# Performance work log

Hardware: AMD Instinct MI355X
Metric: run time of the kernel (lower is better)

## Reference

```python
import jax, jax.numpy as jnp
import numpy as np
from math import sqrt

B, C, L = 32, 32, 512            # batch, channels(enc_in), seq_len
INTRA, INTER = 1024, 256          # memory-bank intra_len, inter_len
DCP, DDE = 64, 512                # compress width (retrieved set size), denoise hidden
SCALE = 0.05


def setup_inputs() -> dict:
    key = jax.random.key(0)
    ks = jax.random.split(key, 12)
    s = 0.02  # small init scale for weights
    return {
        "x_loc": jax.random.normal(ks[0], (B, C, L), jnp.float32),
        "indices": jax.random.randint(ks[1], (B, L), 0, INTRA),
        "map_raw": jax.random.normal(ks[2], (C, INTRA, INTER), jnp.float32),
        # compress: Linear(INTER->DCP), ReLU, Linear(DCP->DCP)
        "cW1": jax.random.normal(ks[3], (DCP, INTER), jnp.float32) * s,
        "cb1": jnp.zeros((DCP,), jnp.float32),
        "cW2": jax.random.normal(ks[4], (DCP, DCP), jnp.float32) * s,
        "cb2": jnp.zeros((DCP,), jnp.float32),
        # denoise: Linear(INTRA->DDE), ReLU, Linear(DDE->INTRA)
        "dW1": jax.random.normal(ks[5], (DDE, INTRA), jnp.float32) * s,
        "db1": jnp.zeros((DDE,), jnp.float32),
        "dW2": jax.random.normal(ks[6], (INTRA, DDE), jnp.float32) * s,
        "db2": jnp.zeros((INTRA,), jnp.float32),
        "lamda1": jnp.zeros((C, 1), jnp.float32),
        "lamda2": jnp.zeros((1, L), jnp.float32),
    }


def reference(x_loc, indices, map_raw, cW1, cb1, cW2, cb2,
              dW1, db1, dW2, db2, lamda1, lamda2):
    # compress along inter_len: (C, INTRA, INTER) -> (C, INTRA, DCP)
    map_tmp = jax.nn.relu(map_raw @ cW1.T + cb1) @ cW2.T + cb2
    map_tmp = jnp.swapaxes(map_tmp, 1, 2)            # (C, DCP, INTRA)
    # denoise along intra_len
    map_st = jax.nn.relu(map_tmp @ dW1.T + db1) @ dW2.T + db2  # (C, DCP, INTRA)
    # gather: map_dy[b,c,d,l] = map_st[c, d, indices[b,l]]
    map_dy = jnp.transpose(map_st[:, :, indices], (2, 0, 1, 3))  # (B, C, DCP, L)
    # l1 similarity (negative L1 distance, scaled by sqrt(L))
    scores = -jnp.sum(jnp.abs(x_loc[:, :, None, :] - map_dy), axis=-1) / sqrt(L)  # (B,C,DCP)
    scores = jax.nn.softmax(scores * SCALE, axis=2)
    lamda = jax.nn.sigmoid(lamda1) @ jax.nn.sigmoid(lamda2)     # (C, L)
    x_global = jnp.einsum('bchl,bch->bcl', map_dy, scores)      # (B, C, L)
    return x_global * lamda + x_loc * (1.0 - lamda)
```

## Files before the change

### kernel.cpp

```cpp
#include <hip/hip_runtime.h>
#include <hip/hip_bf16.h>

#define Bn 32
#define Cn 32
#define Ln 512
#define INTRA 1024
#define INTER 256
#define DCP 64
#define DDE 512
#define SCALEF 0.05f

typedef __attribute__((ext_vector_type(8))) short short8;
typedef __attribute__((ext_vector_type(4))) float floatx4;

__device__ __forceinline__ short bf16_of(float f) {
    union { float f; unsigned u; } v; v.f = f;
    unsigned r = (v.u + 0x7FFFu + ((v.u >> 16) & 1u)) >> 16;
    return (short)r;
}
__device__ __forceinline__ float f_of_bf16(short h) {
    union { unsigned u; float f; } v;
    v.u = ((unsigned)(unsigned short)h) << 16;
    return v.f;
}
__device__ __forceinline__ short8 cvt8(float4 a, float4 b) {
    short8 r;
    r[0] = bf16_of(a.x); r[1] = bf16_of(a.y); r[2] = bf16_of(a.z); r[3] = bf16_of(a.w);
    r[4] = bf16_of(b.x); r[5] = bf16_of(b.y); r[6] = bf16_of(b.z); r[7] = bf16_of(b.w);
    return r;
}

__global__ __launch_bounds__(256) void compress_fused(
    const float* __restrict__ map_raw, const float* __restrict__ cW1,
    const float* __restrict__ cb1, const float* __restrict__ cW2,
    const float* __restrict__ cb2, short* __restrict__ M1T)
{
    const int c  = blockIdx.y;
    const int m0 = blockIdx.x * 64;
    const float* A = map_raw + ((long)c * INTRA + m0) * INTER;

    __shared__ short Asb[64 * 72];
    __shared__ short Bsb[64 * 72];
    __shared__ short Tsb[64 * 72];

    const int t = threadIdx.x, w = t >> 6, lane = t & 63;
    const int ln = lane & 15, quad = lane >> 4;
    const int sr = t >> 2, sk = (t & 3) * 16;

    const float* ap = A + sr * INTER + sk;
    const float* bp = cW1 + sr * INTER + sk;

    floatx4 acc[4] = {};
    float4 a0 = *(const float4*)(ap),     a1 = *(const float4*)(ap + 4);
    float4 a2 = *(const float4*)(ap + 8), a3 = *(const float4*)(ap + 12);
    float4 b0 = *(const float4*)(bp),     b1 = *(const float4*)(bp + 4);
    float4 b2 = *(const float4*)(bp + 8), b3 = *(const float4*)(bp + 12);

    for (int k0 = 0; k0 < INTER; k0 += 64) {
        __syncthreads();
        *(short8*)&Asb[sr * 72 + sk]     = cvt8(a0, a1);
        *(short8*)&Asb[sr * 72 + sk + 8] = cvt8(a2, a3);
        *(short8*)&Bsb[sr * 72 + sk]     = cvt8(b0, b1);
        *(short8*)&Bsb[sr * 72 + sk + 8] = cvt8(b2, b3);
        __syncthreads();
        const int kn = k0 + 64;
        if (kn < INTER) {
            a0 = *(const float4*)(ap + kn);     a1 = *(const float4*)(ap + kn + 4);
            a2 = *(const float4*)(ap + kn + 8); a3 = *(const float4*)(ap + kn + 12);
            b0 = *(const float4*)(bp + kn);     b1 = *(const float4*)(bp + kn + 4);
            b2 = *(const float4*)(bp + kn + 8); b3 = *(const float4*)(bp + kn + 12);
        }
        #pragma unroll
        for (int kc = 0; kc < 2; ++kc) {
            short8 af = *(const short8*)&Asb[(w * 16 + ln) * 72 + kc * 32 + quad * 8];
            #pragma unroll
            for (int nt = 0; nt < 4; ++nt) {
                short8 bf = *(const short8*)&Bsb[(nt * 16 + ln) * 72 + kc * 32 + quad * 8];
                acc[nt] = __builtin_amdgcn_mfma_f32_16x16x32_bf16(af, bf, acc[nt], 0, 0, 0);
            }
        }
    }
    __syncthreads();

    #pragma unroll
    for (int nt = 0; nt < 4; ++nt) {
        const int n = nt * 16 + ln;
        const float b = cb1[n];
        #pragma unroll
        for (int r = 0; r < 4; ++r)
            Tsb[(w * 16 + quad * 4 + r) * 72 + n] = bf16_of(fmaxf(acc[nt][r] + b, 0.f));
    }
    __syncthreads();

    floatx4 acc2[4] = {};
    #pragma unroll
    for (int ks = 0; ks < 2; ++ks) {
        short8 af = *(const short8*)&Tsb[(w * 16 + ln) * 72 + ks * 32 + quad * 8];
        #pragma unroll
        for (int nt = 0; nt < 4; ++nt) {
            const float* wp = cW2 + (nt * 16 + ln) * 64 + ks * 32 + quad * 8;
            short8 bf = cvt8(*(const float4*)wp, *(const float4*)(wp + 4));
            acc2[nt] = __builtin_amdgcn_mfma_f32_16x16x32_bf16(af, bf, acc2[nt], 0, 0, 0);
        }
    }

    short* outp = M1T + (long)c * 64 * INTRA;
    #pragma unroll
    for (int nt = 0; nt < 4; ++nt) {
        const int n = nt * 16 + ln;
        const float b = cb2[n];
        short t0 = bf16_of(acc2[nt][0] + b);
        short t1 = bf16_of(acc2[nt][1] + b);
        short t2 = bf16_of(acc2[nt][2] + b);
        short t3 = bf16_of(acc2[nt][3] + b);
        *(short4*)(outp + (long)n * INTRA + m0 + w * 16 + quad * 4) =
            make_short4(t0, t1, t2, t3);
    }
}

__global__ __launch_bounds__(256) void gemm_dn1(
    const float* __restrict__ dW1, const short* __restrict__ M1T,
    const float* __restrict__ db1, short* __restrict__ HT)
{
    const int c  = blockIdx.y;
    const int h0 = blockIdx.x * 32;

    __shared__ short Asb[32 * 136];
    __shared__ short Bsb[64 * 136];

    const int t = threadIdx.x, w = t >> 6, lane = t & 63;
    const int ln = lane & 15, quad = lane >> 4;
    const int ar = t >> 3, ak = (t & 7) * 16;
    const int br = t >> 2, bk = (t & 3) * 32;

    const float* Ap = dW1 + (long)(h0 + ar) * INTRA + ak;
    const short* Bp = M1T + (long)c * 64 * INTRA + (long)br * INTRA + bk;

    floatx4 acc[2] = {};
    float4 fa0 = *(const float4*)(Ap),     fa1 = *(const float4*)(Ap + 4);
    float4 fa2 = *(const float4*)(Ap + 8), fa3 = *(const float4*)(Ap + 12);
    short8 sb0 = *(const short8*)(Bp),      sb1 = *(const short8*)(Bp + 8);
    short8 sb2 = *(const short8*)(Bp + 16), sb3 = *(const short8*)(Bp + 24);

    const int mb = (w & 1) * 16;
    const int nb = (w >> 1) * 2;

    for (int k0 = 0; k0 < INTRA; k0 += 128) {
        __syncthreads();
        *(short8*)&Asb[ar * 136 + ak]      = cvt8(fa0, fa1);
        *(short8*)&Asb[ar * 136 + ak + 8]  = cvt8(fa2, fa3);
        *(short8*)&Bsb[br * 136 + bk]      = sb0;
        *(short8*)&Bsb[br * 136 + bk + 8]  = sb1;
        *(short8*)&Bsb[br * 136 + bk + 16] = sb2;
        *(short8*)&Bsb[br * 136 + bk + 24] = sb3;
        __syncthreads();
        const int kn = k0 + 128;
        if (kn < INTRA) {
            fa0 = *(const float4*)(Ap + kn);     fa1 = *(const float4*)(Ap + kn + 4);
            fa2 = *(const float4*)(Ap + kn + 8); fa3 = *(const float4*)(Ap + kn + 12);
            sb0 = *(const short8*)(Bp + kn);      sb1 = *(const short8*)(Bp + kn + 8);
            sb2 = *(const short8*)(Bp + kn + 16); sb3 = *(const short8*)(Bp + kn + 24);
        }
        #pragma unroll
        for (int kc = 0; kc < 4; ++kc) {
            short8 af  = *(const short8*)&Asb[(mb + ln) * 136 + kc * 32 + quad * 8];
            short8 bf0 = *(const short8*)&Bsb[((nb + 0) * 16 + ln) * 136 + kc * 32 + quad * 8];
            short8 bf1 = *(const short8*)&Bsb[((nb + 1) * 16 + ln) * 136 + kc * 32 + quad * 8];
            acc[0] = __builtin_amdgcn_mfma_f32_16x16x32_bf16(af, bf0, acc[0], 0, 0, 0);
            acc[1] = __builtin_amdgcn_mfma_f32_16x16x32_bf16(af, bf1, acc[1], 0, 0, 0);
        }
    }

    float bm[4];
    #pragma unroll
    for (int r = 0; r < 4; ++r) bm[r] = db1[h0 + mb + quad * 4 + r];

    short* outp = HT + (long)c * 64 * DDE;
    #pragma unroll
    for (int j = 0; j < 2; ++j) {
        const int d = (nb + j) * 16 + ln;
        float v0 = fmaxf(acc[j][0] + bm[0], 0.f);
        float v1 = fmaxf(acc[j][1] + bm[1], 0.f);
        float v2 = fmaxf(acc[j][2] + bm[2], 0.f);
        float v3 = fmaxf(acc[j][3] + bm[3], 0.f);
        *(short4*)(outp + (long)d * DDE + h0 + mb + quad * 4) =
            make_short4(bf16_of(v0), bf16_of(v1), bf16_of(v2), bf16_of(v3));
    }
}

__global__ __launch_bounds__(256) void gemm_dn2(
    const short* __restrict__ HT, const float* __restrict__ dW2,
    const float* __restrict__ db2, short* __restrict__ S16)
{
    const int c  = blockIdx.y;
    const int n0 = blockIdx.x * 64;

    __shared__ short Asb[64 * 136];
    __shared__ short Bsb[64 * 136];

    const int t = threadIdx.x, w = t >> 6, lane = t & 63;
    const int ln = lane & 15, quad = lane >> 4;
    const int ar = t >> 2, ak = (t & 3) * 32;

    const short* Ap = HT + (long)c * 64 * DDE + (long)ar * DDE + ak;
    const float* Bp = dW2 + (long)(n0 + ar) * DDE + ak;

    floatx4 acc[4] = {};
    short8 sa0 = *(const short8*)(Ap),      sa1 = *(const short8*)(Ap + 8);
    short8 sa2 = *(const short8*)(Ap + 16), sa3 = *(const short8*)(Ap + 24);
    float4 fb0 = *(const float4*)(Bp),      fb1 = *(const float4*)(Bp + 4);
    float4 fb2 = *(const float4*)(Bp + 8),  fb3 = *(const float4*)(Bp + 12);
    float4 fb4 = *(const float4*)(Bp + 16), fb5 = *(const float4*)(Bp + 20);
    float4 fb6 = *(const float4*)(Bp + 24), fb7 = *(const float4*)(Bp + 28);

    for (int k0 = 0; k0 < DDE; k0 += 128) {
        __syncthreads();
        *(short8*)&Asb[ar * 136 + ak]      = sa0;
        *(short8*)&Asb[ar * 136 + ak + 8]  = sa1;
        *(short8*)&Asb[ar * 136 + ak + 16] = sa2;
        *(short8*)&Asb[ar * 136 + ak + 24] = sa3;
        *(short8*)&Bsb[ar * 136 + ak]      = cvt8(fb0, fb1);
        *(short8*)&Bsb[ar * 136 + ak + 8]  = cvt8(fb2, fb3);
        *(short8*)&Bsb[ar * 136 + ak + 16] = cvt8(fb4, fb5);
        *(short8*)&Bsb[ar * 136 + ak + 24] = cvt8(fb6, fb7);
        __syncthreads();
        const int kn = k0 + 128;
        if (kn < DDE) {
            sa0 = *(const short8*)(Ap + kn);      sa1 = *(const short8*)(Ap + kn + 8);
            sa2 = *(const short8*)(Ap + kn + 16); sa3 = *(const short8*)(Ap + kn + 24);
            fb0 = *(const float4*)(Bp + kn);      fb1 = *(const float4*)(Bp + kn + 4);
            fb2 = *(const float4*)(Bp + kn + 8);  fb3 = *(const float4*)(Bp + kn + 12);
            fb4 = *(const float4*)(Bp + kn + 16); fb5 = *(const float4*)(Bp + kn + 20);
            fb6 = *(const float4*)(Bp + kn + 24); fb7 = *(const float4*)(Bp + kn + 28);
        }
        #pragma unroll
        for (int kc = 0; kc < 4; ++kc) {
            short8 af = *(const short8*)&Asb[(w * 16 + ln) * 136 + kc * 32 + quad * 8];
            #pragma unroll
            for (int nt = 0; nt < 4; ++nt) {
                short8 bf = *(const short8*)&Bsb[(nt * 16 + ln) * 136 + kc * 32 + quad * 8];
                acc[nt] = __builtin_amdgcn_mfma_f32_16x16x32_bf16(af, bf, acc[nt], 0, 0, 0);
            }
        }
    }

    const int d0 = w * 16 + quad * 4;
    #pragma unroll
    for (int nt = 0; nt < 4; ++nt) {
        const int i = n0 + nt * 16 + ln;
        const float bb = db2[i];
        short t0 = bf16_of(acc[nt][0] + bb);
        short t1 = bf16_of(acc[nt][1] + bb);
        short t2 = bf16_of(acc[nt][2] + bb);
        short t3 = bf16_of(acc[nt][3] + bb);
        *(short4*)(S16 + ((long)c * INTRA + i) * DCP + d0) = make_short4(t0, t1, t2, t3);
    }
}

__global__ __launch_bounds__(256) void fuse_kernel(
    const float* __restrict__ x_loc, const int* __restrict__ indices,
    const short* __restrict__ S16, const float* __restrict__ lamda1,
    const float* __restrict__ lamda2, float* __restrict__ out)
{
    const int c = blockIdx.x;
    const int b = blockIdx.y;

    __shared__ float xs[Ln];
    __shared__ int   idx[Ln];
    __shared__ float red[4][DCP];
    __shared__ short wbf[DCP];
    __shared__ float ob[Ln];

    const int t = threadIdx.x;
    const float* xp = x_loc + ((long)b * Cn + c) * Ln;
    const int*   ip = indices + (long)b * Ln;
    ((float2*)xs)[t] = ((const float2*)xp)[t];
    ((int2*)idx)[t]  = ((const int2*)ip)[t];
    __syncthreads();

    const short* Sc = S16 + (long)c * INTRA * DCP;
    const int lane = t & 63;
    const int w    = t >> 6;
    const int r    = lane >> 4;
    const int dg   = lane & 15;

    float s0 = 0.f, s1 = 0.f, s2 = 0.f, s3 = 0.f;
    #pragma unroll 4
    for (int i = 0; i < 32; ++i) {
        const int lbase = w * 128 + i * 4;
        const int row   = idx[lbase + r];
        short4 g = *(const short4*)(Sc + (long)row * DCP + dg * 4);
        const float x = xs[lbase + r];
        s0 += fabsf(x - f_of_bf16(g.x));
        s1 += fabsf(x - f_of_bf16(g.y));
        s2 += fabsf(x - f_of_bf16(g.z));
        s3 += fabsf(x - f_of_bf16(g.w));
    }
    s0 += __shfl_xor(s0, 16); s0 += __shfl_xor(s0, 32);
    s1 += __shfl_xor(s1, 16); s1 += __shfl_xor(s1, 32);
    s2 += __shfl_xor(s2, 16); s2 += __shfl_xor(s2, 32);
    s3 += __shfl_xor(s3, 16); s3 += __shfl_xor(s3, 32);
    if (lane < 16) {
        red[w][dg * 4 + 0] = s0;
        red[w][dg * 4 + 1] = s1;
        red[w][dg * 4 + 2] = s2;
        red[w][dg * 4 + 3] = s3;
    }
    __syncthreads();

    if (t < DCP) {
        float sc = red[0][t] + red[1][t] + red[2][t] + red[3][t];
        sc = -sc * (SCALEF * 0.044194173824159216f);
        float m = sc;
        #pragma unroll
        for (int o = 32; o > 0; o >>= 1) m = fmaxf(m, __shfl_xor(m, o));
        float e = __expf(sc - m);
        float ssum = e;
        #pragma unroll
        for (int o = 32; o > 0; o >>= 1) ssum += __shfl_xor(ssum, o);
        wbf[t] = bf16_of(e / ssum);
    }
    __syncthreads();

    const int quad = lane >> 4;
    const int ln16 = lane & 15;
    short8 bw0 = *(const short8*)&wbf[quad * 8];
    short8 bw1 = *(const short8*)&wbf[32 + quad * 8];

    #pragma unroll
    for (int mt = 0; mt < 8; ++mt) {
        const int mrow = w * 128 + mt * 16 + ln16;
        const short* rp = Sc + (long)idx[mrow] * DCP;
        short8 a0 = *(const short8*)(rp + quad * 8);
        short8 a1 = *(const short8*)(rp + 32 + quad * 8);
        floatx4 acc = {};
        acc = __builtin_amdgcn_mfma_f32_16x16x32_bf16(a0, bw0, acc, 0, 0, 0);
        acc = __builtin_amdgcn_mfma_f32_16x16x32_bf16(a1, bw1, acc, 0, 0, 0);
        if (ln16 == 0) {
            const int l0 = w * 128 + mt * 16 + quad * 4;
            ob[l0 + 0] = acc[0];
            ob[l0 + 1] = acc[1];
            ob[l0 + 2] = acc[2];
            ob[l0 + 3] = acc[3];
        }
    }
    __syncthreads();

    const float lam1 = 1.f / (1.f + __expf(-lamda1[c]));
    #pragma unroll
    for (int j = 0; j < 2; ++j) {
        const int l = t + j * 256;
        const float lam = lam1 * (1.f / (1.f + __expf(-lamda2[l])));
        out[((long)b * Cn + c) * Ln + l] = ob[l] * lam + xs[l] * (1.f - lam);
    }
}

extern "C" void kernel_launch(void* const* d_in, const int* in_sizes, int n_in,
                              void* d_out, int out_size, void* d_ws, size_t ws_size,
                              hipStream_t stream)
{
    const float* x_loc   = (const float*)d_in[0];
    const int*   indices = (const int*)d_in[1];
    const float* map_raw = (const float*)d_in[2];
    const float* cW1     = (const float*)d_in[3];
    const float* cb1     = (const float*)d_in[4];
    const float* cW2     = (const float*)d_in[5];
    const float* cb2     = (const float*)d_in[6];
    const float* dW1     = (const float*)d_in[7];
    const float* db1     = (const float*)d_in[8];
    const float* dW2     = (const float*)d_in[9];
    const float* db2     = (const float*)d_in[10];
    const float* lamda1  = (const float*)d_in[11];
    const float* lamda2  = (const float*)d_in[12];
    float* out = (float*)d_out;

    short* wsS = (short*)d_ws;
    short* M1T = wsS;
    short* HT  = M1T + 2097152;
    short* S16 = HT + 1048576;

    compress_fused<<<dim3(INTRA / 64, Cn), 256, 0, stream>>>(
        map_raw, cW1, cb1, cW2, cb2, M1T);

    gemm_dn1<<<dim3(DDE / 32, Cn), 256, 0, stream>>>(
        dW1, M1T, db1, HT);

    gemm_dn2<<<dim3(INTRA / 64, Cn), 256, 0, stream>>>(
        HT, dW2, db2, S16);

    fuse_kernel<<<dim3(Cn, Bn), 256, 0, stream>>>(
        x_loc, indices, S16, lamda1, lamda2, out);
}
```

Baseline: 144.8 us.

## Halve GEMM tile sizes for more blocks and cache gathered rows in LDS

Each of the three GEMM kernels (compress, denoise-1, denoise-2) now uses half the output tile per block and launches twice as many blocks, so more workgroups run in parallel across the CUs. The fuse kernel stores the gathered bf16 rows into a swizzled LDS buffer during the L1-distance pass. The MFMA weighted-sum pass then reads those rows from LDS instead of gathering them from global memory a second time. In exchange, weights are reloaded more often across blocks, and the fuse kernel uses about 72KB of LDS, which may reduce occupancy.

```diff
diff --git a/kernel.cpp b/kernel.cpp
--- a/kernel.cpp
+++ b/kernel.cpp
@@ -36,130 +36,49 @@
     const float* __restrict__ cb2, short* __restrict__ M1T)
 {
     const int c  = blockIdx.y;
-    const int m0 = blockIdx.x * 64;
+    const int m0 = blockIdx.x * 32;
     const float* A = map_raw + ((long)c * INTRA + m0) * INTER;
-
-    __shared__ short Asb[64 * 72];
-    __shared__ short Bsb[64 * 72];
-    __shared__ short Tsb[64 * 72];
-
-    const int t = threadIdx.x, w = t >> 6, lane = t & 63;
-    const int ln = lane & 15, quad = lane >> 4;
-    const int sr = t >> 2, sk = (t & 3) * 16;
-
-    const float* ap = A + sr * INTER + sk;
-    const float* bp = cW1 + sr * INTER + sk;
-
-    floatx4 acc[4] = {};
-    float4 a0 = *(const float4*)(ap),     a1 = *(const float4*)(ap + 4);
-    float4 a2 = *(const float4*)(ap + 8), a3 = *(const float4*)(ap + 12);
-    float4 b0 = *(const float4*)(bp),     b1 = *(const float4*)(bp + 4);
-    float4 b2 = *(const float4*)(bp + 8), b3 = *(const float4*)(bp + 12);
-
-    for (int k0 = 0; k0 < INTER; k0 += 64) {
-        __syncthreads();
-        *(short8*)&Asb[sr * 72 + sk]     = cvt8(a0, a1);
-        *(short8*)&Asb[sr * 72 + sk + 8] = cvt8(a2, a3);
-        *(short8*)&Bsb[sr * 72 + sk]     = cvt8(b0, b1);
-        *(short8*)&Bsb[sr * 72 + sk + 8] = cvt8(b2, b3);
-        __syncthreads();
-        const int kn = k0 + 64;
-        if (kn < INTER) {
-            a0 = *(const float4*)(ap + kn);     a1 = *(const float4*)(ap + kn + 4);
-            a2 = *(const float4*)(ap + kn + 8); a3 = *(const float4*)(ap + kn + 12);
-            b0 = *(const float4*)(bp + kn);     b1 = *(const float4*)(bp + kn + 4);
-            b2 = *(const float4*)(bp + kn + 8); b3 = *(const float4*)(bp + kn + 12);
-        }
-        #pragma unroll
-        for (int kc = 0; kc < 2; ++kc) {
-            short8 af = *(const short8*)&Asb[(w * 16 + ln) * 72 + kc * 32 + quad * 8];
-            #pragma unroll
-            for (int nt = 0; nt < 4; ++nt) {
-                short8 bf = *(const short8*)&Bsb[(nt * 16 + ln) * 72 + kc * 32 + quad * 8];
-                acc[nt] = __builtin_amdgcn_mfma_f32_16x16x32_bf16(af, bf, acc[nt], 0, 0, 0);
-            }
-        }
-    }
-    __syncthreads();
-
-    #pragma unroll
-    for (int nt = 0; nt < 4; ++nt) {
-        const int n = nt * 16 + ln;
-        const float b = cb1[n];
-        #pragma unroll
-        for (int r = 0; r < 4; ++r)
-            Tsb[(w * 16 + quad * 4 + r) * 72 + n] = bf16_of(fmaxf(acc[nt][r] + b, 0.f));
-    }
-    __syncthreads();
-
-    floatx4 acc2[4] = {};
-    #pragma unroll
-    for (int ks = 0; ks < 2; ++ks) {
-        short8 af = *(const short8*)&Tsb[(w * 16 + ln) * 72 + ks * 32 + quad * 8];
-        #pragma unroll
-        for (int nt = 0; nt < 4; ++nt) {
-            const float* wp = cW2 + (nt * 16 + ln) * 64 + ks * 32 + quad * 8;
-            short8 bf = cvt8(*(const float4*)wp, *(const float4*)(wp + 4));
-            acc2[nt] = __builtin_amdgcn_mfma_f32_16x16x32_bf16(af, bf, acc2[nt], 0, 0, 0);
-        }
-    }
-
-    short* outp = M1T + (long)c * 64 * INTRA;
-    #pragma unroll
-    for (int nt = 0; nt < 4; ++nt) {
-        const int n = nt * 16 + ln;
-        const float b = cb2[n];
-        short t0 = bf16_of(acc2[nt][0] + b);
-        short t1 = bf16_of(acc2[nt][1] + b);
-        short t2 = bf16_of(acc2[nt][2] + b);
-        short t3 = bf16_of(acc2[nt][3] + b);
-        *(short4*)(outp + (long)n * INTRA + m0 + w * 16 + quad * 4) =
-            make_short4(t0, t1, t2, t3);
-    }
-}
-
-__global__ __launch_bounds__(256) void gemm_dn1(
-    const float* __restrict__ dW1, const short* __restrict__ M1T,
-    const float* __restrict__ db1, short* __restrict__ HT)
-{
-    const int c  = blockIdx.y;
-    const int h0 = blockIdx.x * 32;
 
     __shared__ short Asb[32 * 136];
     __shared__ short Bsb[64 * 136];
+    __shared__ short Tsb[32 * 72];
 
     const int t = threadIdx.x, w = t >> 6, lane = t & 63;
     const int ln = lane & 15, quad = lane >> 4;
     const int ar = t >> 3, ak = (t & 7) * 16;
     const int br = t >> 2, bk = (t & 3) * 32;
 
-    const float* Ap = dW1 + (long)(h0 + ar) * INTRA + ak;
-    const short* Bp = M1T + (long)c * 64 * INTRA + (long)br * INTRA + bk;
-
-    floatx4 acc[2] = {};
-    float4 fa0 = *(const float4*)(Ap),     fa1 = *(const float4*)(Ap + 4);
-    float4 fa2 = *(const float4*)(Ap + 8), fa3 = *(const float4*)(Ap + 12);
-    short8 sb0 = *(const short8*)(Bp),      sb1 = *(const short8*)(Bp + 8);
-    short8 sb2 = *(const short8*)(Bp + 16), sb3 = *(const short8*)(Bp + 24);
+    const float* ap = A + (long)ar * INTER + ak;
+    const float* bp = cW1 + (long)br * INTER + bk;
 
     const int mb = (w & 1) * 16;
     const int nb = (w >> 1) * 2;
 
-    for (int k0 = 0; k0 < INTRA; k0 += 128) {
+    floatx4 acc[2] = {};
+    float4 fa0 = *(const float4*)(ap),      fa1 = *(const float4*)(ap + 4);
+    float4 fa2 = *(const float4*)(ap + 8),  fa3 = *(const float4*)(ap + 12);
+    float4 fb0 = *(const float4*)(bp),      fb1 = *(const float4*)(bp + 4);
+    float4 fb2 = *(const float4*)(bp + 8),  fb3 = *(const float4*)(bp + 12);
+    float4 fb4 = *(const float4*)(bp + 16), fb5 = *(const float4*)(bp + 20);
+    float4 fb6 = *(const float4*)(bp + 24), fb7 = *(const float4*)(bp + 28);
+
+    for (int k0 = 0; k0 < INTER; k0 += 128) {
         __syncthreads();
         *(short8*)&Asb[ar * 136 + ak]      = cvt8(fa0, fa1);
         *(short8*)&Asb[ar * 136 + ak + 8]  = cvt8(fa2, fa3);
-        *(short8*)&Bsb[br * 136 + bk]      = sb0;
-        *(short8*)&Bsb[br * 136 + bk + 8]  = sb1;
-        *(short8*)&Bsb[br * 136 + bk + 16] = sb2;
-        *(short8*)&Bsb[br * 136 + bk + 24] = sb3;
+        *(short8*)&Bsb[br * 136 + bk]      = cvt8(fb0, fb1);
+        *(short8*)&Bsb[br * 136 + bk + 8]  = cvt8(fb2, fb3);
+        *(short8*)&Bsb[br * 136 + bk + 16] = cvt8(fb4, fb5);
+        *(short8*)&Bsb[br * 136 + bk + 24] = cvt8(fb6, fb7);
         __syncthreads();
         const int kn = k0 + 128;
-        if (kn < INTRA) {
-            fa0 = *(const float4*)(Ap + kn);     fa1 = *(const float4*)(Ap + kn + 4);
-            fa2 = *(const float4*)(Ap + kn + 8); fa3 = *(const float4*)(Ap + kn + 12);
-            sb0 = *(const short8*)(Bp + kn);      sb1 = *(const short8*)(Bp + kn + 8);
-            sb2 = *(const short8*)(Bp + kn + 16); sb3 = *(const short8*)(Bp + kn + 24);
+        if (kn < INTER) {
+            fa0 = *(const float4*)(ap + kn);      fa1 = *(const float4*)(ap + kn + 4);
+            fa2 = *(const float4*)(ap + kn + 8);  fa3 = *(const float4*)(ap + kn + 12);
+            fb0 = *(const float4*)(bp + kn);      fb1 = *(const float4*)(bp + kn + 4);
+            fb2 = *(const float4*)(bp + kn + 8);  fb3 = *(const float4*)(bp + kn + 12);
+            fb4 = *(const float4*)(bp + kn + 16); fb5 = *(const float4*)(bp + kn + 20);
+            fb6 = *(const float4*)(bp + kn + 24); fb7 = *(const float4*)(bp + kn + 28);
         }
         #pragma unroll
         for (int kc = 0; kc < 4; ++kc) {
@@ -171,21 +90,98 @@
         }
     }
 
+    #pragma unroll
+    for (int j = 0; j < 2; ++j) {
+        const int n = (nb + j) * 16 + ln;
+        const float b = cb1[n];
+        #pragma unroll
+        for (int r = 0; r < 4; ++r)
+            Tsb[(mb + quad * 4 + r) * 72 + n] = bf16_of(fmaxf(acc[j][r] + b, 0.f));
+    }
+    __syncthreads();
+
+    floatx4 acc2[2] = {};
+    #pragma unroll
+    for (int ks = 0; ks < 2; ++ks) {
+        short8 af = *(const short8*)&Tsb[(mb + ln) * 72 + ks * 32 + quad * 8];
+        #pragma unroll
+        for (int j = 0; j < 2; ++j) {
+            const float* wp = cW2 + ((nb + j) * 16 + ln) * 64 + ks * 32 + quad * 8;
+            short8 bf = cvt8(*(const float4*)wp, *(const float4*)(wp + 4));
+            acc2[j] = __builtin_amdgcn_mfma_f32_16x16x32_bf16(af, bf, acc2[j], 0, 0, 0);
+        }
+    }
+
+    short* outp = M1T + (long)c * 64 * INTRA;
+    const int is = m0 + mb + quad * 4;
+    #pragma unroll
+    for (int j = 0; j < 2; ++j) {
+        const int n = (nb + j) * 16 + ln;
+        const float b = cb2[n];
+        short t0 = bf16_of(acc2[j][0] + b);
+        short t1 = bf16_of(acc2[j][1] + b);
+        short t2 = bf16_of(acc2[j][2] + b);
+        short t3 = bf16_of(acc2[j][3] + b);
+        *(short4*)(outp + (long)n * INTRA + is) = make_short4(t0, t1, t2, t3);
+    }
+}
+
+__global__ __launch_bounds__(256) void gemm_dn1(
+    const float* __restrict__ dW1, const short* __restrict__ M1T,
+    const float* __restrict__ db1, short* __restrict__ HT)
+{
+    const int c  = blockIdx.y;
+    const int h0 = blockIdx.x * 16;
+
+    __shared__ short Asb[16 * 136];
+    __shared__ short Bsb[64 * 136];
+
+    const int t = threadIdx.x, w = t >> 6, lane = t & 63;
+    const int ln = lane & 15, quad = lane >> 4;
+    const int ar = t >> 4, ak = (t & 15) * 8;
+    const int br = t >> 2, bk = (t & 3) * 32;
+
+    const float* Ap = dW1 + (long)(h0 + ar) * INTRA + ak;
+    const short* Bp = M1T + (long)c * 64 * INTRA + (long)br * INTRA + bk;
+
+    floatx4 acc = {};
+    float4 fa0 = *(const float4*)(Ap), fa1 = *(const float4*)(Ap + 4);
+    short8 sb0 = *(const short8*)(Bp),      sb1 = *(const short8*)(Bp + 8);
+    short8 sb2 = *(const short8*)(Bp + 16), sb3 = *(const short8*)(Bp + 24);
+
+    for (int k0 = 0; k0 < INTRA; k0 += 128) {
+        __syncthreads();
+        *(short8*)&Asb[ar * 136 + ak]      = cvt8(fa0, fa1);
+        *(short8*)&Bsb[br * 136 + bk]      = sb0;
+        *(short8*)&Bsb[br * 136 + bk + 8]  = sb1;
+        *(short8*)&Bsb[br * 136 + bk + 16] = sb2;
+        *(short8*)&Bsb[br * 136 + bk + 24] = sb3;
+        __syncthreads();
+        const int kn = k0 + 128;
+        if (kn < INTRA) {
+            fa0 = *(const float4*)(Ap + kn);      fa1 = *(const float4*)(Ap + kn + 4);
+            sb0 = *(const short8*)(Bp + kn);      sb1 = *(const short8*)(Bp + kn + 8);
+            sb2 = *(const short8*)(Bp + kn + 16); sb3 = *(const short8*)(Bp + kn + 24);
+        }
+        #pragma unroll
+        for (int kc = 0; kc < 4; ++kc) {
+            short8 af = *(const short8*)&Asb[ln * 136 + kc * 32 + quad * 8];
+            short8 bf = *(const short8*)&Bsb[(w * 16 + ln) * 136 + kc * 32 + quad * 8];
+            acc = __builtin_amdgcn_mfma_f32_16x16x32_bf16(af, bf, acc, 0, 0, 0);
+        }
+    }
+
     float bm[4];
     #pragma unroll
-    for (int r = 0; r < 4; ++r) bm[r] = db1[h0 + mb + quad * 4 + r];
-
-    short* outp = HT + (long)c * 64 * DDE;
-    #pragma unroll
-    for (int j = 0; j < 2; ++j) {
-        const int d = (nb + j) * 16 + ln;
-        float v0 = fmaxf(acc[j][0] + bm[0], 0.f);
-        float v1 = fmaxf(acc[j][1] + bm[1], 0.f);
-        float v2 = fmaxf(acc[j][2] + bm[2], 0.f);
-        float v3 = fmaxf(acc[j][3] + bm[3], 0.f);
-        *(short4*)(outp + (long)d * DDE + h0 + mb + quad * 4) =
-            make_short4(bf16_of(v0), bf16_of(v1), bf16_of(v2), bf16_of(v3));
-    }
+    for (int r = 0; r < 4; ++r) bm[r] = db1[h0 + quad * 4 + r];
+
+    const int d = w * 16 + ln;
+    float v0 = fmaxf(acc[0] + bm[0], 0.f);
+    float v1 = fmaxf(acc[1] + bm[1], 0.f);
+    float v2 = fmaxf(acc[2] + bm[2], 0.f);
+    float v3 = fmaxf(acc[3] + bm[3], 0.f);
+    *(short4*)(HT + (long)c * 64 * DDE + (long)d * DDE + h0 + quad * 4) =
+        make_short4(bf16_of(v0), bf16_of(v1), bf16_of(v2), bf16_of(v3));
 }
 
 __global__ __launch_bounds__(256) void gemm_dn2(
@@ -193,36 +189,33 @@
     const float* __restrict__ db2, short* __restrict__ S16)
 {
     const int c  = blockIdx.y;
-    const int n0 = blockIdx.x * 64;
+    const int i0 = blockIdx.x * 32;
 
     __shared__ short Asb[64 * 136];
-    __shared__ short Bsb[64 * 136];
+    __shared__ short Bsb[32 * 136];
 
     const int t = threadIdx.x, w = t >> 6, lane = t & 63;
     const int ln = lane & 15, quad = lane >> 4;
-    const int ar = t >> 2, ak = (t & 3) * 32;
-
-    const short* Ap = HT + (long)c * 64 * DDE + (long)ar * DDE + ak;
-    const float* Bp = dW2 + (long)(n0 + ar) * DDE + ak;
-
-    floatx4 acc[4] = {};
+    const int br = t >> 2, bk = (t & 3) * 32;
+    const int ar = t >> 3, ak = (t & 7) * 16;
+
+    const short* Ap = HT + (long)c * 64 * DDE + (long)br * DDE + bk;
+    const float* Bp = dW2 + (long)(i0 + ar) * DDE + ak;
+
+    floatx4 acc[2] = {};
     short8 sa0 = *(const short8*)(Ap),      sa1 = *(const short8*)(Ap + 8);
     short8 sa2 = *(const short8*)(Ap + 16), sa3 = *(const short8*)(Ap + 24);
     float4 fb0 = *(const float4*)(Bp),      fb1 = *(const float4*)(Bp + 4);
     float4 fb2 = *(const float4*)(Bp + 8),  fb3 = *(const float4*)(Bp + 12);
-    float4 fb4 = *(const float4*)(Bp + 16), fb5 = *(const float4*)(Bp + 20);
-    float4 fb6 = *(const float4*)(Bp + 24), fb7 = *(const float4*)(Bp + 28);
 
     for (int k0 = 0; k0 < DDE; k0 += 128) {
         __syncthreads();
-        *(short8*)&Asb[ar * 136 + ak]      = sa0;
-        *(short8*)&Asb[ar * 136 + ak + 8]  = sa1;
-        *(short8*)&Asb[ar * 136 + ak + 16] = sa2;
-        *(short8*)&Asb[ar * 136 + ak + 24] = sa3;
+        *(short8*)&Asb[br * 136 + bk]      = sa0;
+        *(short8*)&Asb[br * 136 + bk + 8]  = sa1;
+        *(short8*)&Asb[br * 136 + bk + 16] = sa2;
+        *(short8*)&Asb[br * 136 + bk + 24] = sa3;
         *(short8*)&Bsb[ar * 136 + ak]      = cvt8(fb0, fb1);
         *(short8*)&Bsb[ar * 136 + ak + 8]  = cvt8(fb2, fb3);
-        *(short8*)&Bsb[ar * 136 + ak + 16] = cvt8(fb4, fb5);
-        *(short8*)&Bsb[ar * 136 + ak + 24] = cvt8(fb6, fb7);
         __syncthreads();
         const int kn = k0 + 128;
         if (kn < DDE) {
@@ -230,29 +223,27 @@
             sa2 = *(const short8*)(Ap + kn + 16); sa3 = *(const short8*)(Ap + kn + 24);
             fb0 = *(const float4*)(Bp + kn);      fb1 = *(const float4*)(Bp + kn + 4);
             fb2 = *(const float4*)(Bp + kn + 8);  fb3 = *(const float4*)(Bp + kn + 12);
-            fb4 = *(const float4*)(Bp + kn + 16); fb5 = *(const float4*)(Bp + kn + 20);
-            fb6 = *(const float4*)(Bp + kn + 24); fb7 = *(const float4*)(Bp + kn + 28);
         }
         #pragma unroll
         for (int kc = 0; kc < 4; ++kc) {
             short8 af = *(const short8*)&Asb[(w * 16 + ln) * 136 + kc * 32 + quad * 8];
             #pragma unroll
-            for (int nt = 0; nt < 4; ++nt) {
-                short8 bf = *(const short8*)&Bsb[(nt * 16 + ln) * 136 + kc * 32 + quad * 8];
-                acc[nt] = __builtin_amdgcn_mfma_f32_16x16x32_bf16(af, bf, acc[nt], 0, 0, 0);
+            for (int j = 0; j < 2; ++j) {
+                short8 bf = *(const short8*)&Bsb[(j * 16 + ln) * 136 + kc * 32 + quad * 8];
+                acc[j] = __builtin_amdgcn_mfma_f32_16x16x32_bf16(af, bf, acc[j], 0, 0, 0);
             }
         }
     }
 
     const int d0 = w * 16 + quad * 4;
     #pragma unroll
-    for (int nt = 0; nt < 4; ++nt) {
-        const int i = n0 + nt * 16 + ln;
+    for (int j = 0; j < 2; ++j) {
+        const int i = i0 + j * 16 + ln;
         const float bb = db2[i];
-        short t0 = bf16_of(acc[nt][0] + bb);
-        short t1 = bf16_of(acc[nt][1] + bb);
-        short t2 = bf16_of(acc[nt][2] + bb);
-        short t3 = bf16_of(acc[nt][3] + bb);
+        short t0 = bf16_of(acc[j][0] + bb);
+        short t1 = bf16_of(acc[j][1] + bb);
+        short t2 = bf16_of(acc[j][2] + bb);
+        short t3 = bf16_of(acc[j][3] + bb);
         *(short4*)(S16 + ((long)c * INTRA + i) * DCP + d0) = make_short4(t0, t1, t2, t3);
     }
 }
@@ -265,11 +256,13 @@
     const int c = blockIdx.x;
     const int b = blockIdx.y;
 
-    __shared__ float xs[Ln];
-    __shared__ int   idx[Ln];
-    __shared__ float red[4][DCP];
-    __shared__ short wbf[DCP];
-    __shared__ float ob[Ln];
+    __shared__ __align__(16) short smem[36416];
+    short* G   = smem;
+    float* xs  = (float*)(smem + 32768);
+    int*   idx = (int*)(smem + 33792);
+    float (*red)[DCP] = (float(*)[DCP])(smem + 34816);
+    short* wbf = smem + 35328;
+    float* ob  = (float*)(smem + 35392);
 
     const int t = threadIdx.x;
     const float* xp = x_loc + ((long)b * Cn + c) * Ln;
@@ -287,10 +280,11 @@
     float s0 = 0.f, s1 = 0.f, s2 = 0.f, s3 = 0.f;
     #pragma unroll 4
     for (int i = 0; i < 32; ++i) {
-        const int lbase = w * 128 + i * 4;
-        const int row   = idx[lbase + r];
+        const int l   = w * 128 + i * 4 + r;
+        const int row = idx[l];
         short4 g = *(const short4*)(Sc + (long)row * DCP + dg * 4);
-        const float x = xs[lbase + r];
+        *(short4*)&G[l * 64 + (((dg >> 1) ^ (l & 7)) * 8) + (dg & 1) * 4] = g;
+        const float x = xs[l];
         s0 += fabsf(x - f_of_bf16(g.x));
         s1 += fabsf(x - f_of_bf16(g.y));
         s2 += fabsf(x - f_of_bf16(g.z));
@@ -330,9 +324,8 @@
     #pragma unroll
     for (int mt = 0; mt < 8; ++mt) {
         const int mrow = w * 128 + mt * 16 + ln16;
-        const short* rp = Sc + (long)idx[mrow] * DCP;
-        short8 a0 = *(const short8*)(rp + quad * 8);
-        short8 a1 = *(const short8*)(rp + 32 + quad * 8);
+        short8 a0 = *(const short8*)&G[mrow * 64 + ((quad ^ (mrow & 7)) * 8)];
+        short8 a1 = *(const short8*)&G[mrow * 64 + (((4 + quad) ^ (mrow & 7)) * 8)];
         floatx4 acc = {};
         acc = __builtin_amdgcn_mfma_f32_16x16x32_bf16(a0, bw0, acc, 0, 0, 0);
         acc = __builtin_amdgcn_mfma_f32_16x16x32_bf16(a1, bw1, acc, 0, 0, 0);
@@ -379,13 +372,13 @@
     short* HT  = M1T + 2097152;
     short* S16 = HT + 1048576;
 
-    compress_fused<<<dim3(INTRA / 64, Cn), 256, 0, stream>>>(
+    compress_fused<<<dim3(INTRA / 32, Cn), 256, 0, stream>>>(
         map_raw, cW1, cb1, cW2, cb2, M1T);
 
-    gemm_dn1<<<dim3(DDE / 32, Cn), 256, 0, stream>>>(
+    gemm_dn1<<<dim3(DDE / 16, Cn), 256, 0, stream>>>(
         dW1, M1T, db1, HT);
 
-    gemm_dn2<<<dim3(INTRA / 64, Cn), 256, 0, stream>>>(
+    gemm_dn2<<<dim3(INTRA / 32, Cn), 256, 0, stream>>>(
         HT, dW2, db2, S16);
 
     fuse_kernel<<<dim3(Cn, Bn), 256, 0, stream>>>(
```

After: 152.8 us. 1.06x slower.

## Fuse denoise GEMMs into one kernel with pre-converted bf16 weights

Applied to the files above, without the earlier changes.

Adds a prep kernel that converts dW1 and dW2 to bf16 once per call. The two denoise GEMM kernels are replaced by one 1024-thread kernel launched as 128 blocks (4 per channel), and each block recomputes the full hidden activation for its channel. The aim is to save a launch and avoid repeated fp32 weight loads and conversions, at the cost of four-fold redundant first-GEMM work per channel. Only 128 large blocks run, so much of the GPU may sit idle.

```diff
diff --git a/kernel.cpp b/kernel.cpp
--- a/kernel.cpp
+++ b/kernel.cpp
@@ -28,6 +28,19 @@
     r[0] = bf16_of(a.x); r[1] = bf16_of(a.y); r[2] = bf16_of(a.z); r[3] = bf16_of(a.w);
     r[4] = bf16_of(b.x); r[5] = bf16_of(b.y); r[6] = bf16_of(b.z); r[7] = bf16_of(b.w);
     return r;
+}
+
+__global__ __launch_bounds__(256) void prep_weights(
+    const float* __restrict__ dW1, const float* __restrict__ dW2,
+    short* __restrict__ dW1b, short* __restrict__ dW2b)
+{
+    const int i = (blockIdx.x * 256 + threadIdx.x) * 8;
+    if (i < DDE * INTRA) {
+        float4 x0 = *(const float4*)(dW1 + i), x1 = *(const float4*)(dW1 + i + 4);
+        *(short8*)(dW1b + i) = cvt8(x0, x1);
+        x0 = *(const float4*)(dW2 + i); x1 = *(const float4*)(dW2 + i + 4);
+        *(short8*)(dW2b + i) = cvt8(x0, x1);
+    }
 }
 
 __global__ __launch_bounds__(256) void compress_fused(
@@ -118,142 +131,130 @@
     }
 }
 
-__global__ __launch_bounds__(256) void gemm_dn1(
-    const float* __restrict__ dW1, const short* __restrict__ M1T,
-    const float* __restrict__ db1, short* __restrict__ HT)
-{
-    const int c  = blockIdx.y;
-    const int h0 = blockIdx.x * 32;
-
-    __shared__ short Asb[32 * 136];
-    __shared__ short Bsb[64 * 136];
-
-    const int t = threadIdx.x, w = t >> 6, lane = t & 63;
+__global__ __launch_bounds__(1024) void dn12(
+    const short* __restrict__ dW1b, const short* __restrict__ dW2b,
+    const short* __restrict__ M1T,
+    const float* __restrict__ db1, const float* __restrict__ db2,
+    short* __restrict__ HTp, short* __restrict__ S16)
+{
+    const int bid = blockIdx.x;
+    const int c   = bid >> 2;
+    const int iq  = bid & 3;
+
+    __shared__ __align__(16) short arena[26112];
+
+    const int t = threadIdx.x;
+    const int w = t >> 6;
+    const int lane = t & 63;
     const int ln = lane & 15, quad = lane >> 4;
-    const int ar = t >> 3, ak = (t & 7) * 16;
-    const int br = t >> 2, bk = (t & 3) * 32;
-
-    const float* Ap = dW1 + (long)(h0 + ar) * INTRA + ak;
-    const short* Bp = M1T + (long)c * 64 * INTRA + (long)br * INTRA + bk;
-
-    floatx4 acc[2] = {};
-    float4 fa0 = *(const float4*)(Ap),     fa1 = *(const float4*)(Ap + 4);
-    float4 fa2 = *(const float4*)(Ap + 8), fa3 = *(const float4*)(Ap + 12);
-    short8 sb0 = *(const short8*)(Bp),      sb1 = *(const short8*)(Bp + 8);
-    short8 sb2 = *(const short8*)(Bp + 16), sb3 = *(const short8*)(Bp + 24);
-
-    const int mb = (w & 1) * 16;
-    const int nb = (w >> 1) * 2;
-
-    for (int k0 = 0; k0 < INTRA; k0 += 128) {
-        __syncthreads();
-        *(short8*)&Asb[ar * 136 + ak]      = cvt8(fa0, fa1);
-        *(short8*)&Asb[ar * 136 + ak + 8]  = cvt8(fa2, fa3);
-        *(short8*)&Bsb[br * 136 + bk]      = sb0;
-        *(short8*)&Bsb[br * 136 + bk + 8]  = sb1;
-        *(short8*)&Bsb[br * 136 + bk + 16] = sb2;
-        *(short8*)&Bsb[br * 136 + bk + 24] = sb3;
-        __syncthreads();
-        const int kn = k0 + 128;
-        if (kn < INTRA) {
-            fa0 = *(const float4*)(Ap + kn);     fa1 = *(const float4*)(Ap + kn + 4);
-            fa2 = *(const float4*)(Ap + kn + 8); fa3 = *(const float4*)(Ap + kn + 12);
-            sb0 = *(const short8*)(Bp + kn);      sb1 = *(const short8*)(Bp + kn + 8);
-            sb2 = *(const short8*)(Bp + kn + 16); sb3 = *(const short8*)(Bp + kn + 24);
-        }
-        #pragma unroll
-        for (int kc = 0; kc < 4; ++kc) {
-            short8 af  = *(const short8*)&Asb[(mb + ln) * 136 + kc * 32 + quad * 8];
-            short8 bf0 = *(const short8*)&Bsb[((nb + 0) * 16 + ln) * 136 + kc * 32 + quad * 8];
-            short8 bf1 = *(const short8*)&Bsb[((nb + 1) * 16 + ln) * 136 + kc * 32 + quad * 8];
-            acc[0] = __builtin_amdgcn_mfma_f32_16x16x32_bf16(af, bf0, acc[0], 0, 0, 0);
-            acc[1] = __builtin_amdgcn_mfma_f32_16x16x32_bf16(af, bf1, acc[1], 0, 0, 0);
-        }
-    }
-
-    float bm[4];
-    #pragma unroll
-    for (int r = 0; r < 4; ++r) bm[r] = db1[h0 + mb + quad * 4 + r];
-
-    short* outp = HT + (long)c * 64 * DDE;
-    #pragma unroll
-    for (int j = 0; j < 2; ++j) {
-        const int d = (nb + j) * 16 + ln;
-        float v0 = fmaxf(acc[j][0] + bm[0], 0.f);
-        float v1 = fmaxf(acc[j][1] + bm[1], 0.f);
-        float v2 = fmaxf(acc[j][2] + bm[2], 0.f);
-        float v3 = fmaxf(acc[j][3] + bm[3], 0.f);
-        *(short4*)(outp + (long)d * DDE + h0 + mb + quad * 4) =
-            make_short4(bf16_of(v0), bf16_of(v1), bf16_of(v2), bf16_of(v3));
-    }
-}
-
-__global__ __launch_bounds__(256) void gemm_dn2(
-    const short* __restrict__ HT, const float* __restrict__ dW2,
-    const float* __restrict__ db2, short* __restrict__ S16)
-{
-    const int c  = blockIdx.y;
-    const int n0 = blockIdx.x * 64;
-
-    __shared__ short Asb[64 * 136];
-    __shared__ short Bsb[64 * 136];
-
-    const int t = threadIdx.x, w = t >> 6, lane = t & 63;
-    const int ln = lane & 15, quad = lane >> 4;
-    const int ar = t >> 2, ak = (t & 3) * 32;
-
-    const short* Ap = HT + (long)c * 64 * DDE + (long)ar * DDE + ak;
-    const float* Bp = dW2 + (long)(n0 + ar) * DDE + ak;
-
-    floatx4 acc[4] = {};
-    short8 sa0 = *(const short8*)(Ap),      sa1 = *(const short8*)(Ap + 8);
-    short8 sa2 = *(const short8*)(Ap + 16), sa3 = *(const short8*)(Ap + 24);
-    float4 fb0 = *(const float4*)(Bp),      fb1 = *(const float4*)(Bp + 4);
-    float4 fb2 = *(const float4*)(Bp + 8),  fb3 = *(const float4*)(Bp + 12);
-    float4 fb4 = *(const float4*)(Bp + 16), fb5 = *(const float4*)(Bp + 20);
-    float4 fb6 = *(const float4*)(Bp + 24), fb7 = *(const float4*)(Bp + 28);
-
-    for (int k0 = 0; k0 < DDE; k0 += 128) {
-        __syncthreads();
-        *(short8*)&Asb[ar * 136 + ak]      = sa0;
-        *(short8*)&Asb[ar * 136 + ak + 8]  = sa1;
-        *(short8*)&Asb[ar * 136 + ak + 16] = sa2;
-        *(short8*)&Asb[ar * 136 + ak + 24] = sa3;
-        *(short8*)&Bsb[ar * 136 + ak]      = cvt8(fb0, fb1);
-        *(short8*)&Bsb[ar * 136 + ak + 8]  = cvt8(fb2, fb3);
-        *(short8*)&Bsb[ar * 136 + ak + 16] = cvt8(fb4, fb5);
-        *(short8*)&Bsb[ar * 136 + ak + 24] = cvt8(fb6, fb7);
-        __syncthreads();
-        const int kn = k0 + 128;
-        if (kn < DDE) {
-            sa0 = *(const short8*)(Ap + kn);      sa1 = *(const short8*)(Ap + kn + 8);
-            sa2 = *(const short8*)(Ap + kn + 16); sa3 = *(const short8*)(Ap + kn + 24);
-            fb0 = *(const float4*)(Bp + kn);      fb1 = *(const float4*)(Bp + kn + 4);
-            fb2 = *(const float4*)(Bp + kn + 8);  fb3 = *(const float4*)(Bp + kn + 12);
-            fb4 = *(const float4*)(Bp + kn + 16); fb5 = *(const float4*)(Bp + kn + 20);
-            fb6 = *(const float4*)(Bp + kn + 24); fb7 = *(const float4*)(Bp + kn + 28);
-        }
-        #pragma unroll
-        for (int kc = 0; kc < 4; ++kc) {
-            short8 af = *(const short8*)&Asb[(w * 16 + ln) * 136 + kc * 32 + quad * 8];
+    const int dt = w & 3;
+    const int tp = (w >> 2) * 2;
+
+    short* Hme = HTp + (long)bid * 64 * DDE;
+
+    {
+        short* Asb = arena;
+        short* Bsb = arena + 17408;
+        const int ar = t >> 3, ak = (t & 7) * 16;
+        const int br = t >> 4, bk = (t & 15) * 8;
+        const short* Bp = M1T + (long)c * 64 * INTRA + (long)br * INTRA + bk;
+
+        for (int hs = 0; hs < 4; ++hs) {
+            const int hb = hs * 128;
+            const short* Ap = dW1b + (long)(hb + ar) * INTRA + ak;
+            floatx4 acc[2] = {};
+            short8 a0 = *(const short8*)(Ap);
+            short8 a1 = *(const short8*)(Ap + 8);
+            short8 b0 = *(const short8*)(Bp);
+
+            for (int k0 = 0; k0 < INTRA; k0 += 128) {
+                __syncthreads();
+                *(short8*)&Asb[ar * 136 + ak]     = a0;
+                *(short8*)&Asb[ar * 136 + ak + 8] = a1;
+                *(short8*)&Bsb[br * 136 + bk]     = b0;
+                __syncthreads();
+                const int kn = k0 + 128;
+                if (kn < INTRA) {
+                    a0 = *(const short8*)(Ap + kn);
+                    a1 = *(const short8*)(Ap + kn + 8);
+                    b0 = *(const short8*)(Bp + kn);
+                }
+                #pragma unroll
+                for (int kc = 0; kc < 4; ++kc) {
+                    short8 bf = *(const short8*)&Bsb[(dt * 16 + ln) * 136 + kc * 32 + quad * 8];
+                    #pragma unroll
+                    for (int j = 0; j < 2; ++j) {
+                        short8 af = *(const short8*)&Asb[((tp + j) * 16 + ln) * 136 + kc * 32 + quad * 8];
+                        acc[j] = __builtin_amdgcn_mfma_f32_16x16x32_bf16(af, bf, acc[j], 0, 0, 0);
+                    }
+                }
+            }
             #pragma unroll
-            for (int nt = 0; nt < 4; ++nt) {
-                short8 bf = *(const short8*)&Bsb[(nt * 16 + ln) * 136 + kc * 32 + quad * 8];
-                acc[nt] = __builtin_amdgcn_mfma_f32_16x16x32_bf16(af, bf, acc[nt], 0, 0, 0);
-            }
-        }
-    }
-
-    const int d0 = w * 16 + quad * 4;
-    #pragma unroll
-    for (int nt = 0; nt < 4; ++nt) {
-        const int i = n0 + nt * 16 + ln;
-        const float bb = db2[i];
-        short t0 = bf16_of(acc[nt][0] + bb);
-        short t1 = bf16_of(acc[nt][1] + bb);
-        short t2 = bf16_of(acc[nt][2] + bb);
-        short t3 = bf16_of(acc[nt][3] + bb);
-        *(short4*)(S16 + ((long)c * INTRA + i) * DCP + d0) = make_short4(t0, t1, t2, t3);
+            for (int j = 0; j < 2; ++j) {
+                const int hrow = hb + (tp + j) * 16 + quad * 4;
+                const int d    = dt * 16 + ln;
+                float v0 = fmaxf(acc[j][0] + db1[hrow + 0], 0.f);
+                float v1 = fmaxf(acc[j][1] + db1[hrow + 1], 0.f);
+                float v2 = fmaxf(acc[j][2] + db1[hrow + 2], 0.f);
+                float v3 = fmaxf(acc[j][3] + db1[hrow + 3], 0.f);
+                *(short4*)(Hme + (long)d * DDE + hrow) =
+                    make_short4(bf16_of(v0), bf16_of(v1), bf16_of(v2), bf16_of(v3));
+            }
+        }
+    }
+    __threadfence();
+    __syncthreads();
+
+    {
+        short* Asb = arena;
+        short* Bsb = arena + 8704;
+        const int ar = t >> 4, ak = (t & 15) * 8;
+        const int br = t >> 3, bk = (t & 7) * 16;
+        const short* Ap = Hme + (long)ar * DDE + ak;
+
+        for (int is = 0; is < 2; ++is) {
+            const int ib = iq * 256 + is * 128;
+            const short* Bp = dW2b + (long)(ib + br) * DDE + bk;
+            floatx4 acc[2] = {};
+            short8 a0 = *(const short8*)(Ap);
+            short8 b0 = *(const short8*)(Bp);
+            short8 b1 = *(const short8*)(Bp + 8);
+
+            for (int k0 = 0; k0 < DDE; k0 += 128) {
+                __syncthreads();
+                *(short8*)&Asb[ar * 136 + ak]     = a0;
+                *(short8*)&Bsb[br * 136 + bk]     = b0;
+                *(short8*)&Bsb[br * 136 + bk + 8] = b1;
+                __syncthreads();
+                const int kn = k0 + 128;
+                if (kn < DDE) {
+                    a0 = *(const short8*)(Ap + kn);
+                    b0 = *(const short8*)(Bp + kn);
+                    b1 = *(const short8*)(Bp + kn + 8);
+                }
+                #pragma unroll
+                for (int kc = 0; kc < 4; ++kc) {
+                    short8 af = *(const short8*)&Asb[(dt * 16 + ln) * 136 + kc * 32 + quad * 8];
+                    #pragma unroll
+                    for (int j = 0; j < 2; ++j) {
+                        short8 bf = *(const short8*)&Bsb[((tp + j) * 16 + ln) * 136 + kc * 32 + quad * 8];
+                        acc[j] = __builtin_amdgcn_mfma_f32_16x16x32_bf16(af, bf, acc[j], 0, 0, 0);
+                    }
+                }
+            }
+            const int d0 = dt * 16 + quad * 4;
+            #pragma unroll
+            for (int j = 0; j < 2; ++j) {
+                const int i = ib + (tp + j) * 16 + ln;
+                const float bb = db2[i];
+                short t0 = bf16_of(acc[j][0] + bb);
+                short t1 = bf16_of(acc[j][1] + bb);
+                short t2 = bf16_of(acc[j][2] + bb);
+                short t3 = bf16_of(acc[j][3] + bb);
+                *(short4*)(S16 + ((long)c * INTRA + i) * DCP + d0) =
+                    make_short4(t0, t1, t2, t3);
+            }
+        }
     }
 }
 
@@ -374,19 +375,19 @@
     const float* lamda2  = (const float*)d_in[12];
     float* out = (float*)d_out;
 
-    short* wsS = (short*)d_ws;
-    short* M1T = wsS;
-    short* HT  = M1T + 2097152;
-    short* S16 = HT + 1048576;
+    short* wsS  = (short*)d_ws;
+    short* M1T  = wsS;
+    short* dW1b = M1T + 2097152;
+    short* dW2b = dW1b + 524288;
+    short* HTp  = dW2b + 524288;
+    short* S16  = HTp + 4194304;
+
+    prep_weights<<<256, 256, 0, stream>>>(dW1, dW2, dW1b, dW2b);
 
     compress_fused<<<dim3(INTRA / 64, Cn), 256, 0, stream>>>(
         map_raw, cW1, cb1, cW2, cb2, M1T);
 
-    gemm_dn1<<<dim3(DDE / 32, Cn), 256, 0, stream>>>(
-        dW1, M1T, db1, HT);
-
-    gemm_dn2<<<dim3(INTRA / 64, Cn), 256, 0, stream>>>(
-        HT, dW2, db2, S16);
+    dn12<<<128, 1024, 0, stream>>>(dW1b, dW2b, M1T, db1, db2, HTp, S16);
 
     fuse_kernel<<<dim3(Cn, Bn), 256, 0, stream>>>(
         x_loc, indices, S16, lamda1, lamda2, out);
```

New measurement: 219.2 us. 1.51x slower.
